# Kernel optimization log

Measured on AMD Instinct MI355X. Metric: run time of the kernel, lower is better.

Reference implementation:

```python
import jax, jax.numpy as jnp
import numpy as np

N_NODES = 50000
N_EDGES = 800000
IN_DIM, HIDDEN, OUT_DIM = 256, 128, 64
N_LAYERS = 2
NEG_SLOPE = 0.1


def setup_inputs() -> dict:
    key = jax.random.key(0)
    ks = jax.random.split(key, 10)
    x = jax.random.normal(ks[0], (N_NODES, IN_DIM), dtype=jnp.float32)
    edge_index = jax.random.randint(ks[1], (2, N_EDGES), 0, N_NODES, dtype=jnp.int64)
    s = 1.0 / np.sqrt(IN_DIM)
    enc_W = jax.random.uniform(ks[2], (IN_DIM, HIDDEN), jnp.float32, -s, s)
    enc_b = jax.random.uniform(ks[3], (HIDDEN,), jnp.float32, -s, s)
    sh = 1.0 / np.sqrt(HIDDEN)
    conv_W = jax.random.uniform(ks[4], (N_LAYERS, HIDDEN, HIDDEN), jnp.float32, -sh, sh)
    conv_b = jnp.zeros((N_LAYERS, HIDDEN), dtype=jnp.float32)
    dec_W = jax.random.uniform(ks[5], (HIDDEN, OUT_DIM), jnp.float32, -sh, sh)
    dec_b = jax.random.uniform(ks[6], (OUT_DIM,), jnp.float32, -sh, sh)
    return {"x": x, "edge_index": edge_index, "enc_W": enc_W, "enc_b": enc_b,
            "conv_W": conv_W, "conv_b": conv_b, "dec_W": dec_W, "dec_b": dec_b}


def _gcn_norm(edge_index, num_nodes):
    # PyG gcn_norm with add_self_loops=True, edge_weight=1
    loops = jnp.arange(num_nodes, dtype=edge_index.dtype)
    src = jnp.concatenate([edge_index[0], loops])
    dst = jnp.concatenate([edge_index[1], loops])
    deg = jax.ops.segment_sum(jnp.ones_like(dst, dtype=jnp.float32), dst,
                              num_segments=num_nodes)
    dinv = jnp.where(deg > 0, jax.lax.rsqrt(deg), 0.0)
    norm = dinv[src] * dinv[dst]  # [E+N]
    return src, dst, norm


def _gcn_conv(h, W, b, src, dst, norm, num_nodes):
    h = h @ W                       # [N, H] dense transform (no bias in lin)
    msg = h[src] * norm[:, None]    # gather + scale, [E+N, H]
    out = jax.ops.segment_sum(msg, dst, num_segments=num_nodes)  # scatter-add
    return out + b


def reference(x, edge_index, enc_W, enc_b, conv_W, conv_b, dec_W, dec_b):
    n = x.shape[0]
    src, dst, norm = _gcn_norm(edge_index, n)
    # eval mode: F.dropout(training=False) is identity
    h = jax.nn.leaky_relu(x @ enc_W + enc_b, NEG_SLOPE)
    for i in range(N_LAYERS):
        h = jax.nn.leaky_relu(_gcn_conv(h, conv_W[i], conv_b[i], src, dst, norm, n),
                              NEG_SLOPE)
    return h @ dec_W + dec_b
```

## Files before the change

kernel.cpp:

```cpp
#include <hip/hip_runtime.h>


constexpr int HID = 128;
constexpr float NEG = 0.1f;
constexpr int CAP = 96;
constexpr int ENC_BLKS = 256;
constexpr int FILL_BLKS = 256;

typedef __attribute__((ext_vector_type(8))) short short8;
typedef __attribute__((ext_vector_type(4))) float f32x4;

union frag8 { short8 s; unsigned u[4]; };

__device__ __forceinline__ float lrelu(float v) { return v > 0.f ? v : v * NEG; }

__device__ __forceinline__ unsigned fbits(float f) {
  union { float f; unsigned u; } c; c.f = f; return c.u;
}
__device__ __forceinline__ unsigned short f2bf(float f) {
  unsigned u = fbits(f);
  return (unsigned short)((u + 0x7fffu + ((u >> 16) & 1u)) >> 16);
}
__device__ __forceinline__ float bf2f(unsigned short h) {
  union { unsigned u; float f; } c; c.u = ((unsigned)h) << 16; return c.f;
}

__global__ __launch_bounds__(256) void k_pre(const float* __restrict__ encW,
                                             const float* __restrict__ convW,
                                             const float* __restrict__ decW,
                                             unsigned short* __restrict__ wf_enc,
                                             unsigned short* __restrict__ wf_c0,
                                             unsigned short* __restrict__ wf_c1,
                                             unsigned short* __restrict__ wf_dec,
                                             int* __restrict__ cursor, int N) {
  if (blockIdx.x < 36) {
    int idx = blockIdx.x * 256 + threadIdx.x;
    const float* W; unsigned short* wf; int WN, NT, base;
    if (idx < 4096)      { W = encW;          wf = wf_enc; WN = 128; NT = 8; base = idx; }
    else if (idx < 6144) { W = convW;         wf = wf_c0;  WN = 128; NT = 8; base = idx - 4096; }
    else if (idx < 8192) { W = convW + 16384; wf = wf_c1;  WN = 128; NT = 8; base = idx - 6144; }
    else if (idx < 9216) { W = decW;          wf = wf_dec; WN = 64;  NT = 4; base = idx - 8192; }
    else return;
    int lane = base & 63, tile = base >> 6;
    int nt = tile % NT, ks = tile / NT;
    int col = nt * 16 + (lane & 15);
    int krow = ks * 32 + (lane >> 4) * 8;
    unsigned short* o = wf + (size_t)base * 16;
#pragma unroll
    for (int j = 0; j < 8; ++j) {
      float v = W[(size_t)(krow + j) * WN + col];
      unsigned short hi = f2bf(v);
      o[j] = hi;
      o[8 + j] = f2bf(v - bf2f(hi));
    }
    return;
  }
  int i = (blockIdx.x - 36) * 256 + threadIdx.x;
  if (i < N) cursor[i] = 0;
}

__global__ __launch_bounds__(256, 2) void k_enc_fill(
    const float* __restrict__ A, const unsigned short* __restrict__ wf,
    const float* __restrict__ bias, const int* __restrict__ src,
    const int* __restrict__ dst, int E, int* __restrict__ cursor,
    unsigned short* __restrict__ eidx2, float* __restrict__ h, int M) {
  if (blockIdx.x >= ENC_BLKS) {
    for (int e = (blockIdx.x - ENC_BLKS) * 256 + threadIdx.x; e < E;
         e += FILL_BLKS * 256) {
      int d = dst[e];
      int pos = atomicAdd(&cursor[d], 1);
      if (pos < CAP) eidx2[(size_t)d * CAP + pos] = (unsigned short)src[e];
    }
    return;
  }
  constexpr int NT = 8, KS = 8, K = 256, N = 128;
  const int wave = threadIdx.x >> 6, lane = threadIdx.x & 63;
  const int q = lane >> 4, c16 = lane & 15;
  const int row0 = blockIdx.x * 256 + wave * 64;
  if (row0 >= M) return;
  const float* ap[4];
#pragma unroll
  for (int m = 0; m < 4; ++m) {
    int r = row0 + m * 16 + c16;
    if (r >= M) r = M - 1;
    ap[m] = A + (size_t)r * K + q * 8;
  }
  f32x4 acc[4][NT];
#pragma unroll
  for (int m = 0; m < 4; ++m)
#pragma unroll
    for (int nt = 0; nt < NT; ++nt) acc[m][nt] = (f32x4){0.f, 0.f, 0.f, 0.f};
  float av[4][8];
#pragma unroll
  for (int m = 0; m < 4; ++m) {
    *(float4*)&av[m][0] = *(const float4*)(ap[m]);
    *(float4*)&av[m][4] = *(const float4*)(ap[m] + 4);
  }
  for (int ks = 0; ks < KS; ++ks) {
    frag8 ahi[4], alo[4];
#pragma unroll
    for (int m = 0; m < 4; ++m) {
      float res[8];
#pragma unroll
      for (int i = 0; i < 8; ++i) {
        union { unsigned u; float f; } t; t.u = fbits(av[m][i]) & 0xffff0000u;
        res[i] = av[m][i] - t.f;
      }
#pragma unroll
      for (int j = 0; j < 4; ++j) {
        ahi[m].u[j] = __builtin_amdgcn_perm(fbits(av[m][2 * j + 1]), fbits(av[m][2 * j]),
                                            0x07060302u);
        alo[m].u[j] = __builtin_amdgcn_perm(fbits(res[2 * j + 1]), fbits(res[2 * j]),
                                            0x07060302u);
      }
    }
    if (ks + 1 < KS) {
#pragma unroll
      for (int m = 0; m < 4; ++m) {
        *(float4*)&av[m][0] = *(const float4*)(ap[m] + (ks + 1) * 32);
        *(float4*)&av[m][4] = *(const float4*)(ap[m] + (ks + 1) * 32 + 4);
      }
    }
    const unsigned short* wp = wf + (size_t)ks * NT * 1024 + lane * 16;
#pragma unroll
    for (int nt = 0; nt < NT; ++nt) {
      short8 bhi = *(const short8*)(wp);
      short8 blo = *(const short8*)(wp + 8);
#pragma unroll
      for (int m = 0; m < 4; ++m) {
        acc[m][nt] = __builtin_amdgcn_mfma_f32_16x16x32_bf16(ahi[m].s, bhi, acc[m][nt], 0, 0, 0);
        acc[m][nt] = __builtin_amdgcn_mfma_f32_16x16x32_bf16(ahi[m].s, blo, acc[m][nt], 0, 0, 0);
        acc[m][nt] = __builtin_amdgcn_mfma_f32_16x16x32_bf16(alo[m].s, bhi, acc[m][nt], 0, 0, 0);
      }
      wp += 1024;
    }
  }
  float bv[NT];
#pragma unroll
  for (int nt = 0; nt < NT; ++nt) bv[nt] = bias[nt * 16 + c16];
#pragma unroll
  for (int m = 0; m < 4; ++m)
#pragma unroll
    for (int r = 0; r < 4; ++r) {
      int gr = row0 + m * 16 + q * 4 + r;
      if (gr >= M) continue;
#pragma unroll
      for (int nt = 0; nt < NT; ++nt)
        h[(size_t)gr * N + nt * 16 + c16] = lrelu(acc[m][nt][r] + bv[nt]);
    }
}

template <int NT, int MODE>
__global__ __launch_bounds__(64, 2) void k_mfma(const float* __restrict__ A,
                                                const unsigned short* __restrict__ wf,
                                                const float* __restrict__ bias,
                                                const int* __restrict__ deg,
                                                void* __restrict__ Cout, int M, int K) {
  const int N = NT * 16;
  const int lane = threadIdx.x;
  const int q = lane >> 4, c16 = lane & 15;
  const int row0 = blockIdx.x * 64;
  const float* ap[4];
#pragma unroll
  for (int m = 0; m < 4; ++m) {
    int r = row0 + m * 16 + c16;
    if (r >= M) r = M - 1;
    ap[m] = A + (size_t)r * K + q * 8;
  }
  f32x4 acc[4][NT];
#pragma unroll
  for (int m = 0; m < 4; ++m)
#pragma unroll
    for (int nt = 0; nt < NT; ++nt) acc[m][nt] = (f32x4){0.f, 0.f, 0.f, 0.f};
  const int KS = K >> 5;
  float av[4][8];
#pragma unroll
  for (int m = 0; m < 4; ++m) {
    *(float4*)&av[m][0] = *(const float4*)(ap[m]);
    *(float4*)&av[m][4] = *(const float4*)(ap[m] + 4);
  }
  for (int ks = 0; ks < KS; ++ks) {
    frag8 ahi[4], alo[4];
#pragma unroll
    for (int m = 0; m < 4; ++m) {
      float res[8];
#pragma unroll
      for (int i = 0; i < 8; ++i) {
        union { unsigned u; float f; } t; t.u = fbits(av[m][i]) & 0xffff0000u;
        res[i] = av[m][i] - t.f;
      }
#pragma unroll
      for (int j = 0; j < 4; ++j) {
        ahi[m].u[j] = __builtin_amdgcn_perm(fbits(av[m][2 * j + 1]), fbits(av[m][2 * j]),
                                            0x07060302u);
        alo[m].u[j] = __builtin_amdgcn_perm(fbits(res[2 * j + 1]), fbits(res[2 * j]),
                                            0x07060302u);
      }
    }
    if (ks + 1 < KS) {
#pragma unroll
      for (int m = 0; m < 4; ++m) {
        *(float4*)&av[m][0] = *(const float4*)(ap[m] + (ks + 1) * 32);
        *(float4*)&av[m][4] = *(const float4*)(ap[m] + (ks + 1) * 32 + 4);
      }
    }
    const unsigned short* wp = wf + (size_t)ks * NT * 1024 + lane * 16;
#pragma unroll
    for (int nt = 0; nt < NT; ++nt) {
      short8 bhi = *(const short8*)(wp);
      short8 blo = *(const short8*)(wp + 8);
#pragma unroll
      for (int m = 0; m < 4; ++m) {
        acc[m][nt] = __builtin_amdgcn_mfma_f32_16x16x32_bf16(ahi[m].s, bhi, acc[m][nt], 0, 0, 0);
        acc[m][nt] = __builtin_amdgcn_mfma_f32_16x16x32_bf16(ahi[m].s, blo, acc[m][nt], 0, 0, 0);
        acc[m][nt] = __builtin_amdgcn_mfma_f32_16x16x32_bf16(alo[m].s, bhi, acc[m][nt], 0, 0, 0);
      }
      wp += 1024;
    }
  }
  float bv[NT];
  if (MODE == 2) {
#pragma unroll
    for (int nt = 0; nt < NT; ++nt) bv[nt] = bias[nt * 16 + c16];
  }
#pragma unroll
  for (int m = 0; m < 4; ++m)
#pragma unroll
    for (int r = 0; r < 4; ++r) {
      int gr = row0 + m * 16 + q * 4 + r;
      if (gr >= M) continue;
      if (MODE == 1) {
        float dv = rsqrtf((float)deg[gr] + 1.0f);
#pragma unroll
        for (int nt = 0; nt < NT; ++nt)
          ((unsigned short*)Cout)[(size_t)gr * N + nt * 16 + c16] =
              f2bf(acc[m][nt][r] * dv);
      } else {
#pragma unroll
        for (int nt = 0; nt < NT; ++nt)
          ((float*)Cout)[(size_t)gr * N + nt * 16 + c16] = acc[m][nt][r] + bv[nt];
      }
    }
}

__global__ __launch_bounds__(256) void k_gather(const int* __restrict__ deg,
                                                const unsigned short* __restrict__ eidx2,
                                                const unsigned short* __restrict__ t,
                                                const float* __restrict__ bias,
                                                float* __restrict__ h, int N) {
  int node = (blockIdx.x * 256 + threadIdx.x) >> 4;
  int lane = threadIdx.x & 15;
  if (node >= N) return;
  const uint4* t4 = (const uint4*)t;
  int dtrue = deg[node];
  int d = dtrue > CAP ? CAP : dtrue;
  const unsigned short* ep = eidx2 + (size_t)node * CAP;
  float acc[8] = {};
#define ADDV(v)                                         \
  {                                                     \
    unsigned dw[4] = {(v).x, (v).y, (v).z, (v).w};      \
    _Pragma("unroll") for (int i = 0; i < 4; ++i) {     \
      union { unsigned u; float f; } lo, hi;            \
      lo.u = dw[i] << 16;                               \
      hi.u = dw[i] & 0xffff0000u;                       \
      acc[2 * i] += lo.f;                               \
      acc[2 * i + 1] += hi.f;                           \
    }                                                   \
  }
  {
    uint4 vs = t4[(size_t)node * 16 + lane];
    ADDV(vs);
  }
  int e = 0;
  for (; e + 8 <= d; e += 8) {
    int4 sa = *(const int4*)(ep + e);
    unsigned s0 = (unsigned)sa.x & 0xffffu, s1 = (unsigned)sa.x >> 16;
    unsigned s2 = (unsigned)sa.y & 0xffffu, s3 = (unsigned)sa.y >> 16;
    unsigned s4 = (unsigned)sa.z & 0xffffu, s5 = (unsigned)sa.z >> 16;
    unsigned s6 = (unsigned)sa.w & 0xffffu, s7 = (unsigned)sa.w >> 16;
    uint4 v0 = t4[(size_t)s0 * 16 + lane];
    uint4 v1 = t4[(size_t)s1 * 16 + lane];
    uint4 v2 = t4[(size_t)s2 * 16 + lane];
    uint4 v3 = t4[(size_t)s3 * 16 + lane];
    uint4 v4 = t4[(size_t)s4 * 16 + lane];
    uint4 v5 = t4[(size_t)s5 * 16 + lane];
    uint4 v6 = t4[(size_t)s6 * 16 + lane];
    uint4 v7 = t4[(size_t)s7 * 16 + lane];
    ADDV(v0); ADDV(v1); ADDV(v2); ADDV(v3);
    ADDV(v4); ADDV(v5); ADDV(v6); ADDV(v7);
  }
  for (; e < d; ++e) {
    unsigned s = ep[e];
    uint4 v = t4[(size_t)s * 16 + lane];
    ADDV(v);
  }
#undef ADDV
  float w = rsqrtf((float)dtrue + 1.0f);
  float* hp = h + (size_t)node * HID + lane * 8;
  const float* bp = bias + lane * 8;
  float4 o1, o2;
  float* o = (float*)&o1;
#pragma unroll
  for (int i = 0; i < 4; ++i) o[i] = lrelu(acc[i] * w + bp[i]);
  o = (float*)&o2;
#pragma unroll
  for (int i = 0; i < 4; ++i) o[i] = lrelu(acc[4 + i] * w + bp[4 + i]);
  *(float4*)hp = o1;
  *(float4*)(hp + 4) = o2;
}

extern "C" void kernel_launch(void* const* d_in, const int* in_sizes, int n_in,
                              void* d_out, int out_size, void* d_ws, size_t ws_size,
                              hipStream_t stream) {
  const float* x = (const float*)d_in[0];
  const int* ei = (const int*)d_in[1];
  const float* enc_W = (const float*)d_in[2];
  const float* enc_b = (const float*)d_in[3];
  const float* conv_W = (const float*)d_in[4];
  const float* conv_b = (const float*)d_in[5];
  const float* dec_W = (const float*)d_in[6];
  const float* dec_b = (const float*)d_in[7];
  float* out = (float*)d_out;

  const int IN_DIM = 256;
  const int N = in_sizes[0] / IN_DIM;
  const int E = in_sizes[1] / 2;
  const int* src = ei;
  const int* dst = ei + E;

  char* wp = (char*)d_ws;
  auto alloc = [&](size_t bytes) {
    void* p = wp;
    wp += (bytes + 255) & ~(size_t)255;
    return p;
  };
  int* cursor = (int*)alloc((size_t)N * 4);
  unsigned short* eidx2 = (unsigned short*)alloc((size_t)N * CAP * 2);
  float* h = (float*)alloc((size_t)N * HID * 4);
  unsigned short* t = (unsigned short*)alloc((size_t)N * HID * 2);
  unsigned short* wf_enc = (unsigned short*)alloc((size_t)8 * 8 * 64 * 16 * 2);
  unsigned short* wf_c0 = (unsigned short*)alloc((size_t)4 * 8 * 64 * 16 * 2);
  unsigned short* wf_c1 = (unsigned short*)alloc((size_t)4 * 8 * 64 * 16 * 2);
  unsigned short* wf_dec = (unsigned short*)alloc((size_t)4 * 4 * 64 * 16 * 2);

  k_pre<<<36 + (N + 255) / 256, 256, 0, stream>>>(enc_W, conv_W, dec_W, wf_enc, wf_c0,
                                                  wf_c1, wf_dec, cursor, N);

  k_enc_fill<<<ENC_BLKS + FILL_BLKS, 256, 0, stream>>>(x, wf_enc, enc_b, src, dst, E,
                                                       cursor, eidx2, h, N);

  const int gm = (N + 63) / 64;
  for (int l = 0; l < 2; ++l) {
    const unsigned short* wf = l ? wf_c1 : wf_c0;
    k_mfma<8, 1><<<gm, 64, 0, stream>>>(h, wf, nullptr, cursor, t, N, HID);
    k_gather<<<(N * 16 + 255) / 256, 256, 0, stream>>>(
        cursor, eidx2, t, conv_b + (size_t)l * HID, h, N);
  }

  k_mfma<4, 2><<<gm, 64, 0, stream>>>(h, wf_dec, dec_b, nullptr, out, N, HID);
}
```

Baseline: 281.2 us.

## Stage pre-split weight fragments in LDS and shrink per-wave row tiles

The dense GEMM kernels (encoder, conv transforms, decoder) now copy the bf16 hi/lo weight fragments into shared memory with global_load_lds, then have 8 waves per 512-thread block read B fragments from LDS. Each wave now handles 16 rows instead of 64, so it needs fewer accumulator registers and more blocks run at once. The encoder loads its 128KB of weights in two halves of 64KB, separated by a barrier. This trades repeated global/L2 weight reads and register pressure for an LDS fill and barriers in every block, and the large LDS footprint may cap how many blocks fit on a CU.

New measurement: 247.2 us. 12.1% less time.

```diff
diff --git a/kernel.cpp b/kernel.cpp
--- a/kernel.cpp
+++ b/kernel.cpp
@@ -4,7 +4,6 @@
 constexpr int HID = 128;
 constexpr float NEG = 0.1f;
 constexpr int CAP = 96;
-constexpr int ENC_BLKS = 256;
 constexpr int FILL_BLKS = 256;
 
 typedef __attribute__((ext_vector_type(8))) short short8;
@@ -23,6 +22,11 @@
 }
 __device__ __forceinline__ float bf2f(unsigned short h) {
   union { unsigned u; float f; } c; c.u = ((unsigned)h) << 16; return c.f;
+}
+
+__device__ __forceinline__ void gload16(const unsigned short* g, unsigned short* l) {
+  __builtin_amdgcn_global_load_lds((const __attribute__((address_space(1))) unsigned*)g,
+                                   (__attribute__((address_space(3))) unsigned*)l, 16, 0, 0);
 }
 
 __global__ __launch_bounds__(256) void k_pre(const float* __restrict__ encW,
@@ -59,162 +63,144 @@
   if (i < N) cursor[i] = 0;
 }
 
-__global__ __launch_bounds__(256, 2) void k_enc_fill(
+__global__ __launch_bounds__(512) void k_enc_fill(
     const float* __restrict__ A, const unsigned short* __restrict__ wf,
     const float* __restrict__ bias, const int* __restrict__ src,
     const int* __restrict__ dst, int E, int* __restrict__ cursor,
-    unsigned short* __restrict__ eidx2, float* __restrict__ h, int M) {
-  if (blockIdx.x >= ENC_BLKS) {
-    for (int e = (blockIdx.x - ENC_BLKS) * 256 + threadIdx.x; e < E;
-         e += FILL_BLKS * 256) {
+    unsigned short* __restrict__ eidx2, float* __restrict__ h, int M, int encB) {
+  __shared__ unsigned short lwf[32768];
+  if (blockIdx.x >= encB) {
+    for (int e = (blockIdx.x - encB) * 512 + threadIdx.x; e < E;
+         e += FILL_BLKS * 512) {
       int d = dst[e];
       int pos = atomicAdd(&cursor[d], 1);
       if (pos < CAP) eidx2[(size_t)d * CAP + pos] = (unsigned short)src[e];
     }
     return;
   }
-  constexpr int NT = 8, KS = 8, K = 256, N = 128;
+  constexpr int NT = 8;
   const int wave = threadIdx.x >> 6, lane = threadIdx.x & 63;
   const int q = lane >> 4, c16 = lane & 15;
-  const int row0 = blockIdx.x * 256 + wave * 64;
-  if (row0 >= M) return;
-  const float* ap[4];
-#pragma unroll
-  for (int m = 0; m < 4; ++m) {
-    int r = row0 + m * 16 + c16;
-    if (r >= M) r = M - 1;
-    ap[m] = A + (size_t)r * K + q * 8;
-  }
-  f32x4 acc[4][NT];
-#pragma unroll
-  for (int m = 0; m < 4; ++m)
-#pragma unroll
-    for (int nt = 0; nt < NT; ++nt) acc[m][nt] = (f32x4){0.f, 0.f, 0.f, 0.f};
-  float av[4][8];
-#pragma unroll
-  for (int m = 0; m < 4; ++m) {
-    *(float4*)&av[m][0] = *(const float4*)(ap[m]);
-    *(float4*)&av[m][4] = *(const float4*)(ap[m] + 4);
-  }
+  const int row0 = blockIdx.x * 128 + wave * 16;
+  int r = row0 + c16;
+  if (r >= M) r = M - 1;
+  const float* ap = A + (size_t)r * 256 + q * 8;
+  f32x4 acc[NT];
+#pragma unroll
+  for (int nt = 0; nt < NT; ++nt) acc[nt] = (f32x4){0.f, 0.f, 0.f, 0.f};
+  float av[8];
+  *(float4*)&av[0] = *(const float4*)(ap);
+  *(float4*)&av[4] = *(const float4*)(ap + 4);
+  for (int half = 0; half < 2; ++half) {
+    if (half) __syncthreads();
+#pragma unroll
+    for (int i = 0; i < 8; ++i) {
+      int c = wave + i * 8;
+      gload16(wf + (size_t)half * 32768 + c * 512 + lane * 8, lwf + c * 512);
+    }
+    asm volatile("s_waitcnt vmcnt(0)" ::: "memory");
+    __syncthreads();
+    for (int ksl = 0; ksl < 4; ++ksl) {
+      frag8 ahi, alo;
+      float res[8];
+#pragma unroll
+      for (int i = 0; i < 8; ++i) {
+        union { unsigned u; float f; } t; t.u = fbits(av[i]) & 0xffff0000u;
+        res[i] = av[i] - t.f;
+      }
+#pragma unroll
+      for (int j = 0; j < 4; ++j) {
+        ahi.u[j] = __builtin_amdgcn_perm(fbits(av[2 * j + 1]), fbits(av[2 * j]),
+                                         0x07060302u);
+        alo.u[j] = __builtin_amdgcn_perm(fbits(res[2 * j + 1]), fbits(res[2 * j]),
+                                         0x07060302u);
+      }
+      int ks = half * 4 + ksl;
+      if (ks + 1 < 8) {
+        *(float4*)&av[0] = *(const float4*)(ap + (ks + 1) * 32);
+        *(float4*)&av[4] = *(const float4*)(ap + (ks + 1) * 32 + 4);
+      }
+      const unsigned short* wp = lwf + ksl * NT * 1024 + lane * 16;
+#pragma unroll
+      for (int nt = 0; nt < NT; ++nt) {
+        short8 bhi = *(const short8*)(wp);
+        short8 blo = *(const short8*)(wp + 8);
+        acc[nt] = __builtin_amdgcn_mfma_f32_16x16x32_bf16(ahi.s, bhi, acc[nt], 0, 0, 0);
+        acc[nt] = __builtin_amdgcn_mfma_f32_16x16x32_bf16(ahi.s, blo, acc[nt], 0, 0, 0);
+        acc[nt] = __builtin_amdgcn_mfma_f32_16x16x32_bf16(alo.s, bhi, acc[nt], 0, 0, 0);
+        wp += 1024;
+      }
+    }
+  }
+  float bv[NT];
+#pragma unroll
+  for (int nt = 0; nt < NT; ++nt) bv[nt] = bias[nt * 16 + c16];
+#pragma unroll
+  for (int rr = 0; rr < 4; ++rr) {
+    int gr = row0 + q * 4 + rr;
+    if (gr >= M) continue;
+#pragma unroll
+    for (int nt = 0; nt < NT; ++nt)
+      h[(size_t)gr * 128 + nt * 16 + c16] = lrelu(acc[nt][rr] + bv[nt]);
+  }
+}
+
+template <int NT, int KS, int MODE>
+__global__ __launch_bounds__(512) void k_mfma(const float* __restrict__ A,
+                                              const unsigned short* __restrict__ wf,
+                                              const float* __restrict__ bias,
+                                              const int* __restrict__ deg,
+                                              void* __restrict__ Cout, int M) {
+  constexpr int K = KS * 32;
+  constexpr int NOUT = NT * 16;
+  constexpr int CH = KS * NT * 2;
+  __shared__ unsigned short lwf[KS * NT * 1024];
+  const int wave = threadIdx.x >> 6, lane = threadIdx.x & 63;
+  const int q = lane >> 4, c16 = lane & 15;
+  const int row0 = blockIdx.x * 128 + wave * 16;
+  int r = row0 + c16;
+  if (r >= M) r = M - 1;
+  const float* ap = A + (size_t)r * K + q * 8;
+  f32x4 acc[NT];
+#pragma unroll
+  for (int nt = 0; nt < NT; ++nt) acc[nt] = (f32x4){0.f, 0.f, 0.f, 0.f};
+  float av[8];
+  *(float4*)&av[0] = *(const float4*)(ap);
+  *(float4*)&av[4] = *(const float4*)(ap + 4);
+#pragma unroll
+  for (int i = 0; i < CH / 8; ++i) {
+    int c = wave + i * 8;
+    gload16(wf + c * 512 + lane * 8, lwf + c * 512);
+  }
+  asm volatile("s_waitcnt vmcnt(0)" ::: "memory");
+  __syncthreads();
   for (int ks = 0; ks < KS; ++ks) {
-    frag8 ahi[4], alo[4];
-#pragma unroll
-    for (int m = 0; m < 4; ++m) {
-      float res[8];
-#pragma unroll
-      for (int i = 0; i < 8; ++i) {
-        union { unsigned u; float f; } t; t.u = fbits(av[m][i]) & 0xffff0000u;
-        res[i] = av[m][i] - t.f;
-      }
-#pragma unroll
-      for (int j = 0; j < 4; ++j) {
-        ahi[m].u[j] = __builtin_amdgcn_perm(fbits(av[m][2 * j + 1]), fbits(av[m][2 * j]),
-                                            0x07060302u);
-        alo[m].u[j] = __builtin_amdgcn_perm(fbits(res[2 * j + 1]), fbits(res[2 * j]),
-                                            0x07060302u);
-      }
+    frag8 ahi, alo;
+    float res[8];
+#pragma unroll
+    for (int i = 0; i < 8; ++i) {
+      union { unsigned u; float f; } t; t.u = fbits(av[i]) & 0xffff0000u;
+      res[i] = av[i] - t.f;
+    }
+#pragma unroll
+    for (int j = 0; j < 4; ++j) {
+      ahi.u[j] = __builtin_amdgcn_perm(fbits(av[2 * j + 1]), fbits(av[2 * j]),
+                                       0x07060302u);
+      alo.u[j] = __builtin_amdgcn_perm(fbits(res[2 * j + 1]), fbits(res[2 * j]),
+                                       0x07060302u);
     }
     if (ks + 1 < KS) {
-#pragma unroll
-      for (int m = 0; m < 4; ++m) {
-        *(float4*)&av[m][0] = *(const float4*)(ap[m] + (ks + 1) * 32);
-        *(float4*)&av[m][4] = *(const float4*)(ap[m] + (ks + 1) * 32 + 4);
-      }
-    }
-    const unsigned short* wp = wf + (size_t)ks * NT * 1024 + lane * 16;
+      *(float4*)&av[0] = *(const float4*)(ap + (ks + 1) * 32);
+      *(float4*)&av[4] = *(const float4*)(ap + (ks + 1) * 32 + 4);
+    }
+    const unsigned short* wp = lwf + ks * NT * 1024 + lane * 16;
 #pragma unroll
     for (int nt = 0; nt < NT; ++nt) {
       short8 bhi = *(const short8*)(wp);
       short8 blo = *(const short8*)(wp + 8);
-#pragma unroll
-      for (int m = 0; m < 4; ++m) {
-        acc[m][nt] = __builtin_amdgcn_mfma_f32_16x16x32_bf16(ahi[m].s, bhi, acc[m][nt], 0, 0, 0);
-        acc[m][nt] = __builtin_amdgcn_mfma_f32_16x16x32_bf16(ahi[m].s, blo, acc[m][nt], 0, 0, 0);
-        acc[m][nt] = __builtin_amdgcn_mfma_f32_16x16x32_bf16(alo[m].s, bhi, acc[m][nt], 0, 0, 0);
-      }
-      wp += 1024;
-    }
-  }
-  float bv[NT];
-#pragma unroll
-  for (int nt = 0; nt < NT; ++nt) bv[nt] = bias[nt * 16 + c16];
-#pragma unroll
-  for (int m = 0; m < 4; ++m)
-#pragma unroll
-    for (int r = 0; r < 4; ++r) {
-      int gr = row0 + m * 16 + q * 4 + r;
-      if (gr >= M) continue;
-#pragma unroll
-      for (int nt = 0; nt < NT; ++nt)
-        h[(size_t)gr * N + nt * 16 + c16] = lrelu(acc[m][nt][r] + bv[nt]);
-    }
-}
-
-template <int NT, int MODE>
-__global__ __launch_bounds__(64, 2) void k_mfma(const float* __restrict__ A,
-                                                const unsigned short* __restrict__ wf,
-                                                const float* __restrict__ bias,
-                                                const int* __restrict__ deg,
-                                                void* __restrict__ Cout, int M, int K) {
-  const int N = NT * 16;
-  const int lane = threadIdx.x;
-  const int q = lane >> 4, c16 = lane & 15;
-  const int row0 = blockIdx.x * 64;
-  const float* ap[4];
-#pragma unroll
-  for (int m = 0; m < 4; ++m) {
-    int r = row0 + m * 16 + c16;
-    if (r >= M) r = M - 1;
-    ap[m] = A + (size_t)r * K + q * 8;
-  }
-  f32x4 acc[4][NT];
-#pragma unroll
-  for (int m = 0; m < 4; ++m)
-#pragma unroll
-    for (int nt = 0; nt < NT; ++nt) acc[m][nt] = (f32x4){0.f, 0.f, 0.f, 0.f};
-  const int KS = K >> 5;
-  float av[4][8];
-#pragma unroll
-  for (int m = 0; m < 4; ++m) {
-    *(float4*)&av[m][0] = *(const float4*)(ap[m]);
-    *(float4*)&av[m][4] = *(const float4*)(ap[m] + 4);
-  }
-  for (int ks = 0; ks < KS; ++ks) {
-    frag8 ahi[4], alo[4];
-#pragma unroll
-    for (int m = 0; m < 4; ++m) {
-      float res[8];
-#pragma unroll
-      for (int i = 0; i < 8; ++i) {
-        union { unsigned u; float f; } t; t.u = fbits(av[m][i]) & 0xffff0000u;
-        res[i] = av[m][i] - t.f;
-      }
-#pragma unroll
-      for (int j = 0; j < 4; ++j) {
-        ahi[m].u[j] = __builtin_amdgcn_perm(fbits(av[m][2 * j + 1]), fbits(av[m][2 * j]),
-                                            0x07060302u);
-        alo[m].u[j] = __builtin_amdgcn_perm(fbits(res[2 * j + 1]), fbits(res[2 * j]),
-                                            0x07060302u);
-      }
-    }
-    if (ks + 1 < KS) {
-#pragma unroll
-      for (int m = 0; m < 4; ++m) {
-        *(float4*)&av[m][0] = *(const float4*)(ap[m] + (ks + 1) * 32);
-        *(float4*)&av[m][4] = *(const float4*)(ap[m] + (ks + 1) * 32 + 4);
-      }
-    }
-    const unsigned short* wp = wf + (size_t)ks * NT * 1024 + lane * 16;
-#pragma unroll
-    for (int nt = 0; nt < NT; ++nt) {
-      short8 bhi = *(const short8*)(wp);
-      short8 blo = *(const short8*)(wp + 8);
-#pragma unroll
-      for (int m = 0; m < 4; ++m) {
-        acc[m][nt] = __builtin_amdgcn_mfma_f32_16x16x32_bf16(ahi[m].s, bhi, acc[m][nt], 0, 0, 0);
-        acc[m][nt] = __builtin_amdgcn_mfma_f32_16x16x32_bf16(ahi[m].s, blo, acc[m][nt], 0, 0, 0);
-        acc[m][nt] = __builtin_amdgcn_mfma_f32_16x16x32_bf16(alo[m].s, bhi, acc[m][nt], 0, 0, 0);
-      }
+      acc[nt] = __builtin_amdgcn_mfma_f32_16x16x32_bf16(ahi.s, bhi, acc[nt], 0, 0, 0);
+      acc[nt] = __builtin_amdgcn_mfma_f32_16x16x32_bf16(ahi.s, blo, acc[nt], 0, 0, 0);
+      acc[nt] = __builtin_amdgcn_mfma_f32_16x16x32_bf16(alo.s, bhi, acc[nt], 0, 0, 0);
       wp += 1024;
     }
   }
@@ -224,23 +210,21 @@
     for (int nt = 0; nt < NT; ++nt) bv[nt] = bias[nt * 16 + c16];
   }
 #pragma unroll
-  for (int m = 0; m < 4; ++m)
-#pragma unroll
-    for (int r = 0; r < 4; ++r) {
-      int gr = row0 + m * 16 + q * 4 + r;
-      if (gr >= M) continue;
-      if (MODE == 1) {
-        float dv = rsqrtf((float)deg[gr] + 1.0f);
-#pragma unroll
-        for (int nt = 0; nt < NT; ++nt)
-          ((unsigned short*)Cout)[(size_t)gr * N + nt * 16 + c16] =
-              f2bf(acc[m][nt][r] * dv);
-      } else {
-#pragma unroll
-        for (int nt = 0; nt < NT; ++nt)
-          ((float*)Cout)[(size_t)gr * N + nt * 16 + c16] = acc[m][nt][r] + bv[nt];
-      }
-    }
+  for (int rr = 0; rr < 4; ++rr) {
+    int gr = row0 + q * 4 + rr;
+    if (gr >= M) continue;
+    if (MODE == 1) {
+      float dv = rsqrtf((float)deg[gr] + 1.0f);
+#pragma unroll
+      for (int nt = 0; nt < NT; ++nt)
+        ((unsigned short*)Cout)[(size_t)gr * NOUT + nt * 16 + c16] =
+            f2bf(acc[nt][rr] * dv);
+    } else {
+#pragma unroll
+      for (int nt = 0; nt < NT; ++nt)
+        ((float*)Cout)[(size_t)gr * NOUT + nt * 16 + c16] = acc[nt][rr] + bv[nt];
+    }
+  }
 }
 
 __global__ __launch_bounds__(256) void k_gather(const int* __restrict__ deg,
@@ -346,16 +330,17 @@
   k_pre<<<36 + (N + 255) / 256, 256, 0, stream>>>(enc_W, conv_W, dec_W, wf_enc, wf_c0,
                                                   wf_c1, wf_dec, cursor, N);
 
-  k_enc_fill<<<ENC_BLKS + FILL_BLKS, 256, 0, stream>>>(x, wf_enc, enc_b, src, dst, E,
-                                                       cursor, eidx2, h, N);
-
-  const int gm = (N + 63) / 64;
+  const int encB = (N + 127) / 128;
+  k_enc_fill<<<encB + FILL_BLKS, 512, 0, stream>>>(x, wf_enc, enc_b, src, dst, E,
+                                                   cursor, eidx2, h, N, encB);
+
+  const int gm = (N + 127) / 128;
   for (int l = 0; l < 2; ++l) {
     const unsigned short* wf = l ? wf_c1 : wf_c0;
-    k_mfma<8, 1><<<gm, 64, 0, stream>>>(h, wf, nullptr, cursor, t, N, HID);
+    k_mfma<8, 4, 1><<<gm, 512, 0, stream>>>(h, wf, nullptr, cursor, t, N);
     k_gather<<<(N * 16 + 255) / 256, 256, 0, stream>>>(
         cursor, eidx2, t, conv_b + (size_t)l * HID, h, N);
   }
 
-  k_mfma<4, 2><<<gm, 64, 0, stream>>>(h, wf_dec, dec_b, nullptr, out, N, HID);
-}
+  k_mfma<4, 4, 2><<<gm, 512, 0, stream>>>(h, wf_dec, dec_b, nullptr, out, N);
+}
```
